# Kernel tuning notes

Hardware: AMD Instinct MI355X
Metric: run time of the kernel (lower is better)

Reference implementation:

```python
import jax, jax.numpy as jnp
import numpy as np

B, N, D, E, R = 4, 65536, 256, 1536, 512

def setup_inputs() -> dict:
    key = jax.random.key(0)
    k0, k1, k2, k3 = jax.random.split(key, 4)
    canvas = jax.random.normal(k0, (B, N, D), dtype=jnp.float32)
    embeddings = jax.random.normal(k1, (R, E), dtype=jnp.float32)  # frozen semantic embeddings
    W = jax.random.normal(k2, (D, E), dtype=jnp.float32) * 0.02    # projector weight (out, in)
    residuals = jnp.zeros((R, D), dtype=jnp.float32)               # zero-init learned residuals
    region_ids = jax.random.randint(k3, (N,), 0, R, dtype=jnp.int32)  # per-position region map from layout
    return {"canvas": canvas, "embeddings": embeddings, "W": W, "residuals": residuals, "region_ids": region_ids}

def reference(canvas, embeddings, W, residuals, region_ids):
    # get_all_conditioning: project embeddings to d_model and add residuals
    all_cond = jnp.einsum('re,de->rd', embeddings, W) + residuals  # [R, D]
    # condition_canvas: the per-region loop is a gather of all_cond by region id,
    # broadcast over batch and added to the canvas in one fused pass.
    return canvas + all_cond[region_ids][None]  # [B, N, D]
```

## Files before the change

### kernel.cpp

```cpp
#include <hip/hip_runtime.h>


#define B_DIM 4
#define N_DIM 65536
#define D_DIM 256
#define E_DIM 1536
#define R_DIM 512
#define RPB   8
#define KS    8
#define KSUB  (E_DIM / KS)
#define KSUB4 (KSUB / 4)

typedef float f32x4 __attribute__((ext_vector_type(4)));

__global__ __launch_bounds__(256) void k_transpose(const float* __restrict__ W,
                                                   float* __restrict__ Wt) {
    __shared__ float t[32][33];
    const int eb = blockIdx.x * 32;
    const int db = blockIdx.y * 32;
    const int tx = threadIdx.x & 31;
    const int ty = threadIdx.x >> 5;
#pragma unroll
    for (int j = 0; j < 4; ++j)
        t[ty + 8 * j][tx] = W[(size_t)(db + ty + 8 * j) * E_DIM + eb + tx];
    __syncthreads();
#pragma unroll
    for (int j = 0; j < 4; ++j)
        Wt[(size_t)(eb + ty + 8 * j) * D_DIM + db + tx] = t[tx][ty + 8 * j];
}

__global__ __launch_bounds__(256) void k_cond_part(const float* __restrict__ emb,
                                                   const float* __restrict__ Wt,
                                                   float* __restrict__ part) {
    __shared__ f32x4 embs[RPB][KSUB4];
    const int r0 = blockIdx.x * RPB;
    const int ks = blockIdx.y;
    const int d  = threadIdx.x;

    const f32x4* eg = reinterpret_cast<const f32x4*>(emb);
    for (int f = d; f < RPB * KSUB4; f += 256) {
        const int rr = f / KSUB4, gg = f % KSUB4;
        embs[rr][gg] = eg[(size_t)(r0 + rr) * (E_DIM / 4) + ks * KSUB4 + gg];
    }
    __syncthreads();

    float a0 = 0.f, a1 = 0.f, a2 = 0.f, a3 = 0.f;
    float a4 = 0.f, a5 = 0.f, a6 = 0.f, a7 = 0.f;
    const int ebase = ks * KSUB;
#pragma unroll 4
    for (int g = 0; g < KSUB4; ++g) {
        const int e = ebase + 4 * g;
        const float w0 = Wt[(size_t)(e + 0) * D_DIM + d];
        const float w1 = Wt[(size_t)(e + 1) * D_DIM + d];
        const float w2 = Wt[(size_t)(e + 2) * D_DIM + d];
        const float w3 = Wt[(size_t)(e + 3) * D_DIM + d];
        { const f32x4 v = embs[0][g]; a0 += v.x*w0 + v.y*w1 + v.z*w2 + v.w*w3; }
        { const f32x4 v = embs[1][g]; a1 += v.x*w0 + v.y*w1 + v.z*w2 + v.w*w3; }
        { const f32x4 v = embs[2][g]; a2 += v.x*w0 + v.y*w1 + v.z*w2 + v.w*w3; }
        { const f32x4 v = embs[3][g]; a3 += v.x*w0 + v.y*w1 + v.z*w2 + v.w*w3; }
        { const f32x4 v = embs[4][g]; a4 += v.x*w0 + v.y*w1 + v.z*w2 + v.w*w3; }
        { const f32x4 v = embs[5][g]; a5 += v.x*w0 + v.y*w1 + v.z*w2 + v.w*w3; }
        { const f32x4 v = embs[6][g]; a6 += v.x*w0 + v.y*w1 + v.z*w2 + v.w*w3; }
        { const f32x4 v = embs[7][g]; a7 += v.x*w0 + v.y*w1 + v.z*w2 + v.w*w3; }
    }
    float* p = part + ((size_t)ks * R_DIM + r0) * D_DIM + d;
    p[0 * D_DIM] = a0;
    p[1 * D_DIM] = a1;
    p[2 * D_DIM] = a2;
    p[3 * D_DIM] = a3;
    p[4 * D_DIM] = a4;
    p[5 * D_DIM] = a5;
    p[6 * D_DIM] = a6;
    p[7 * D_DIM] = a7;
}

__global__ __launch_bounds__(256) void k_reduce(const float* __restrict__ part,
                                                const float* __restrict__ res,
                                                float* __restrict__ cond) {
    const int i = blockIdx.x * 256 + threadIdx.x;
    const size_t stride = (size_t)R_DIM * D_DIM;
    float s = res[i];
#pragma unroll
    for (int ks = 0; ks < KS; ++ks)
        s += part[i + ks * stride];
    cond[i] = s;
}

__global__ __launch_bounds__(256) void k_add(const f32x4* __restrict__ canvas,
                                             const int* __restrict__ rid,
                                             const f32x4* __restrict__ cond,
                                             f32x4* __restrict__ out) {
    const int i = blockIdx.x * blockDim.x + threadIdx.x;
    const int n  = (i >> 6) & (N_DIM - 1);
    const int d4 = i & 63;
    const f32x4 c = canvas[i];
    const int r  = rid[n];
    const f32x4 a = cond[r * (D_DIM / 4) + d4];
    __builtin_nontemporal_store(c + a, &out[i]);
}

extern "C" void kernel_launch(void* const* d_in, const int* in_sizes, int n_in,
                              void* d_out, int out_size, void* d_ws, size_t ws_size,
                              hipStream_t stream) {
    const float* canvas = (const float*)d_in[0];
    const float* emb    = (const float*)d_in[1];
    const float* W      = (const float*)d_in[2];
    const float* res    = (const float*)d_in[3];
    const int*   rid    = (const int*)d_in[4];

    float* Wt   = (float*)d_ws;
    float* part = Wt + (size_t)E_DIM * D_DIM;
    float* cond = part + (size_t)KS * R_DIM * D_DIM;

    dim3 tgrid(E_DIM / 32, D_DIM / 32);
    k_transpose<<<tgrid, 256, 0, stream>>>(W, Wt);
    dim3 cgrid(R_DIM / RPB, KS);
    k_cond_part<<<cgrid, 256, 0, stream>>>(emb, Wt, part);
    k_reduce<<<(R_DIM * D_DIM) / 256, 256, 0, stream>>>(part, res, cond);
    k_add<<<(B_DIM * N_DIM * (D_DIM / 4)) / 256, 256, 0, stream>>>(
        (const f32x4*)canvas, rid, (const f32x4*)cond, (f32x4*)d_out);
}
```

Before: 117.6 us.

## Drop W transpose kernel and batch-loop the broadcast add over four batches

Removes the separate transpose kernel and has the projection kernel read W rows directly as float4 along E, which drops one launch and the Wt round trip. The cost is strided per-thread row reads of W, which no longer coalesce across the wavefront. The add kernel now processes all four batch slices per thread, so the region-id lookup and conditioning gather happen once per position instead of four times. The grid shrinks by a factor of four accordingly.

```diff
diff --git a/kernel.cpp b/kernel.cpp
--- a/kernel.cpp
+++ b/kernel.cpp
@@ -13,25 +13,9 @@
 
 typedef float f32x4 __attribute__((ext_vector_type(4)));
 
-__global__ __launch_bounds__(256) void k_transpose(const float* __restrict__ W,
-                                                   float* __restrict__ Wt) {
-    __shared__ float t[32][33];
-    const int eb = blockIdx.x * 32;
-    const int db = blockIdx.y * 32;
-    const int tx = threadIdx.x & 31;
-    const int ty = threadIdx.x >> 5;
-#pragma unroll
-    for (int j = 0; j < 4; ++j)
-        t[ty + 8 * j][tx] = W[(size_t)(db + ty + 8 * j) * E_DIM + eb + tx];
-    __syncthreads();
-#pragma unroll
-    for (int j = 0; j < 4; ++j)
-        Wt[(size_t)(eb + ty + 8 * j) * D_DIM + db + tx] = t[tx][ty + 8 * j];
-}
-
-__global__ __launch_bounds__(256) void k_cond_part(const float* __restrict__ emb,
-                                                   const float* __restrict__ Wt,
-                                                   float* __restrict__ part) {
+__global__ __launch_bounds__(256) void k_cond_direct(const float* __restrict__ emb,
+                                                     const float* __restrict__ W,
+                                                     float* __restrict__ part) {
     __shared__ f32x4 embs[RPB][KSUB4];
     const int r0 = blockIdx.x * RPB;
     const int ks = blockIdx.y;
@@ -46,14 +30,12 @@
 
     float a0 = 0.f, a1 = 0.f, a2 = 0.f, a3 = 0.f;
     float a4 = 0.f, a5 = 0.f, a6 = 0.f, a7 = 0.f;
-    const int ebase = ks * KSUB;
+    const f32x4* wrow =
+        reinterpret_cast<const f32x4*>(W + (size_t)d * E_DIM + ks * KSUB);
 #pragma unroll 4
     for (int g = 0; g < KSUB4; ++g) {
-        const int e = ebase + 4 * g;
-        const float w0 = Wt[(size_t)(e + 0) * D_DIM + d];
-        const float w1 = Wt[(size_t)(e + 1) * D_DIM + d];
-        const float w2 = Wt[(size_t)(e + 2) * D_DIM + d];
-        const float w3 = Wt[(size_t)(e + 3) * D_DIM + d];
+        const f32x4 w = wrow[g];
+        const float w0 = w.x, w1 = w.y, w2 = w.z, w3 = w.w;
         { const f32x4 v = embs[0][g]; a0 += v.x*w0 + v.y*w1 + v.z*w2 + v.w*w3; }
         { const f32x4 v = embs[1][g]; a1 += v.x*w0 + v.y*w1 + v.z*w2 + v.w*w3; }
         { const f32x4 v = embs[2][g]; a2 += v.x*w0 + v.y*w1 + v.z*w2 + v.w*w3; }
@@ -90,13 +72,20 @@
                                              const int* __restrict__ rid,
                                              const f32x4* __restrict__ cond,
                                              f32x4* __restrict__ out) {
+    const int bstep = N_DIM * (D_DIM / 4);
     const int i = blockIdx.x * blockDim.x + threadIdx.x;
-    const int n  = (i >> 6) & (N_DIM - 1);
+    const f32x4 c0 = canvas[i];
+    const f32x4 c1 = canvas[i + bstep];
+    const f32x4 c2 = canvas[i + 2 * bstep];
+    const f32x4 c3 = canvas[i + 3 * bstep];
+    const int n  = i >> 6;
     const int d4 = i & 63;
-    const f32x4 c = canvas[i];
     const int r  = rid[n];
     const f32x4 a = cond[r * (D_DIM / 4) + d4];
-    __builtin_nontemporal_store(c + a, &out[i]);
+    __builtin_nontemporal_store(c0 + a, &out[i]);
+    __builtin_nontemporal_store(c1 + a, &out[i + bstep]);
+    __builtin_nontemporal_store(c2 + a, &out[i + 2 * bstep]);
+    __builtin_nontemporal_store(c3 + a, &out[i + 3 * bstep]);
 }
 
 extern "C" void kernel_launch(void* const* d_in, const int* in_sizes, int n_in,
@@ -108,15 +97,12 @@
     const float* res    = (const float*)d_in[3];
     const int*   rid    = (const int*)d_in[4];
 
-    float* Wt   = (float*)d_ws;
-    float* part = Wt + (size_t)E_DIM * D_DIM;
+    float* part = (float*)d_ws;
     float* cond = part + (size_t)KS * R_DIM * D_DIM;
 
-    dim3 tgrid(E_DIM / 32, D_DIM / 32);
-    k_transpose<<<tgrid, 256, 0, stream>>>(W, Wt);
     dim3 cgrid(R_DIM / RPB, KS);
-    k_cond_part<<<cgrid, 256, 0, stream>>>(emb, Wt, part);
+    k_cond_direct<<<cgrid, 256, 0, stream>>>(emb, W, part);
     k_reduce<<<(R_DIM * D_DIM) / 256, 256, 0, stream>>>(part, res, cond);
-    k_add<<<(B_DIM * N_DIM * (D_DIM / 4)) / 256, 256, 0, stream>>>(
-        (const f32x4*)canvas, rid, (const f32x4*)cond, (f32x4*)d_out);
+    k_add<<<16384, 256, 0, stream>>>((const f32x4*)canvas, rid,
+                                     (const f32x4*)cond, (f32x4*)d_out);
 }
```

New measurement: 114.3 us. 1.03x faster.
